# Kernel tuning notes

Hardware: AMD Instinct MI355X
Metric: run time of the kernel (lower is better)

The kernel has to match this reference:

```python
import jax, jax.numpy as jnp
import numpy as np

N_NODES = 50000
N_EDGES = 800000
D_IN = 128
D_OUT = 128


def setup_inputs() -> dict:
    key = jax.random.key(0)
    k1, k2, k3, k4, k5 = jax.random.split(key, 5)
    # xavier-uniform-like scale for the two linear layers (gain for relu ~ sqrt(2))
    bound = float(np.sqrt(2.0) * np.sqrt(6.0 / (D_IN + D_OUT)))
    return {
        "feat": jax.random.normal(k1, (N_NODES, D_IN), dtype=jnp.float32),
        "w_neigh": jax.random.uniform(k2, (D_OUT, D_IN), minval=-bound, maxval=bound, dtype=jnp.float32),
        "w_self": jax.random.uniform(k3, (D_OUT, D_IN), minval=-bound, maxval=bound, dtype=jnp.float32),
        "b_self": jnp.zeros((D_OUT,), dtype=jnp.float32),
        "rows": jax.random.randint(k4, (N_EDGES,), 0, N_NODES, dtype=jnp.int32),  # src node per edge
        "cols": jax.random.randint(k5, (N_EDGES,), 0, N_NODES, dtype=jnp.int32),  # dst node per edge
    }


def reference(feat, w_neigh, w_self, b_self, rows, cols):
    n = feat.shape[0]
    # srcdata = fc_neigh(feat): [N, D_OUT]
    srcdata = feat @ w_neigh.T
    # deg[j] = A.sum(0)[j] = in-degree of destination j (column sums)
    deg = jax.ops.segment_sum(jnp.ones_like(cols, dtype=feat.dtype), cols, num_segments=n)
    # dstdata = (A @ diag(deg)^-1).T @ srcdata  ==  mean over incoming src neighbors
    agg = jax.ops.segment_sum(srcdata[rows], cols, num_segments=n)  # [N, D_OUT]
    dstdata = agg / jnp.where(deg > 0, deg, 1.0)[:, None]
    # rst = fc_self(h_self) + dstdata
    return feat @ w_self.T + b_self + dstdata
```

## Files before the change

kernel.cpp:

```cpp
#include <hip/hip_runtime.h>
#include <hip/hip_bf16.h>

#define D 128
#define CAP 64

typedef __attribute__((ext_vector_type(8))) short bf16x8;
typedef __attribute__((ext_vector_type(4))) float floatx4;

__device__ __forceinline__ unsigned short f2bf(float f) {
    unsigned int u = __float_as_uint(f);
    return (unsigned short)((u + 0x7fffu + ((u >> 16) & 1u)) >> 16);
}

__global__ __launch_bounds__(256) void zero_kernel(int* __restrict__ p, int n) {
    int i = blockIdx.x * 256 + threadIdx.x;
    if (i < n) p[i] = 0;
}

__global__ __launch_bounds__(256) void prep_fill_kernel(
    const float* __restrict__ feat,
    const float* __restrict__ w_self,
    const float* __restrict__ w_neigh,
    const int* __restrict__ rows,
    const int* __restrict__ cols,
    unsigned short* __restrict__ feat_h,
    unsigned short* __restrict__ ws_h,
    unsigned short* __restrict__ wn_h,
    int* __restrict__ cursor,
    unsigned short* __restrict__ slots,
    int n_nodes, int n_edges)
{
    const int b = blockIdx.x;
    const int tid = threadIdx.x;
    const int role = b % 3;

    if (role < 2) {
        int pb = (b / 3) * 2 + role;
        int i  = pb * 256 + tid;
        if (i < n_nodes * 32) {
            float4 v = *(const float4*)&feat[(long long)4 * i];
            ushort4 o;
            o.x = f2bf(v.x); o.y = f2bf(v.y); o.z = f2bf(v.z); o.w = f2bf(v.w);
            *(ushort4*)&feat_h[(long long)4 * i] = o;
        }
    } else {
        int fb = b / 3;
        int e  = fb * 256 + tid;
        if (e < n_edges) {
            int c = cols[e];
            int p = atomicAdd(&cursor[c], 1);
            if (p < CAP) slots[c * CAP + p] = (unsigned short)rows[e];
        }
        if (fb < 32) {
            int i = fb * 256 + tid;
            int j = i & 4095;
            const float* src = (i < 4096) ? w_self : w_neigh;
            unsigned short* dst = (i < 4096) ? ws_h : wn_h;
            float4 v = *(const float4*)&src[4 * j];
            ushort4 o;
            o.x = f2bf(v.x); o.y = f2bf(v.y); o.z = f2bf(v.z); o.w = f2bf(v.w);
            *(ushort4*)&dst[4 * j] = o;
        }
    }
}

__global__ __launch_bounds__(256) void agg_kernel(
    const unsigned short* __restrict__ feat_h,
    const int* __restrict__ cursor,
    const unsigned short* __restrict__ slots,
    unsigned short* __restrict__ agg_h,
    int n_nodes)
{
    int gid = blockIdx.x * 256 + threadIdx.x;
    int node = gid >> 4;
    if (node >= n_nodes) return;
    int q = gid & 15;

    int deg = cursor[node];
    if (deg > CAP) deg = CAP;
    const unsigned short* slot = slots + (long long)node * CAP;

    float acc[8] = {0.f, 0.f, 0.f, 0.f, 0.f, 0.f, 0.f, 0.f};
    if (deg > 0) {
        int r = slot[0];
        for (int k = 0; k < deg; ++k) {
            int rn = (k + 1 < deg) ? (int)slot[k + 1] : 0;
            uint4 v = *(const uint4*)&feat_h[(long long)r * D + q * 8];
            acc[0] += __uint_as_float(v.x << 16);
            acc[1] += __uint_as_float(v.x & 0xffff0000u);
            acc[2] += __uint_as_float(v.y << 16);
            acc[3] += __uint_as_float(v.y & 0xffff0000u);
            acc[4] += __uint_as_float(v.z << 16);
            acc[5] += __uint_as_float(v.z & 0xffff0000u);
            acc[6] += __uint_as_float(v.w << 16);
            acc[7] += __uint_as_float(v.w & 0xffff0000u);
            r = rn;
        }
    }
    float inv = (deg > 0) ? 1.0f / (float)deg : 0.0f;

    ushort4 o0, o1;
    o0.x = f2bf(acc[0] * inv); o0.y = f2bf(acc[1] * inv);
    o0.z = f2bf(acc[2] * inv); o0.w = f2bf(acc[3] * inv);
    o1.x = f2bf(acc[4] * inv); o1.y = f2bf(acc[5] * inv);
    o1.z = f2bf(acc[6] * inv); o1.w = f2bf(acc[7] * inv);
    *(ushort4*)&agg_h[(long long)node * D + q * 8] = o0;
    *(ushort4*)&agg_h[(long long)node * D + q * 8 + 4] = o1;
}

__global__ __launch_bounds__(256) void gemm_mfma(
    const unsigned short* __restrict__ feat_h,
    const unsigned short* __restrict__ agg_h,
    const unsigned short* __restrict__ ws_h,
    const unsigned short* __restrict__ wn_h,
    const float* __restrict__ b_self,
    float* __restrict__ out,
    int n_nodes)
{
    const int tid  = threadIdx.x;
    const int wave = tid >> 6;
    const int lane = tid & 63;
    const int m    = lane & 15;
    const int quad = lane >> 4;
    const int row0 = blockIdx.x * 128 + wave * 32;
    const int kq   = quad * 8;

    floatx4 acc[8][2];
    #pragma unroll
    for (int nt = 0; nt < 8; ++nt)
        #pragma unroll
        for (int h = 0; h < 2; ++h)
            acc[nt][h] = (floatx4){0.f, 0.f, 0.f, 0.f};

    int r0 = row0 + m;      if (r0 > n_nodes - 1) r0 = n_nodes - 1;
    int r1 = row0 + 16 + m; if (r1 > n_nodes - 1) r1 = n_nodes - 1;

    #pragma unroll
    for (int phase = 0; phase < 2; ++phase) {
        const unsigned short* A = phase ? agg_h : feat_h;
        const unsigned short* B = phase ? wn_h : ws_h;
        #pragma unroll
        for (int kt = 0; kt < 4; ++kt) {
            const int k = kt * 32 + kq;
            bf16x8 a0 = *(const bf16x8*)&A[(long long)r0 * D + k];
            bf16x8 a1 = *(const bf16x8*)&A[(long long)r1 * D + k];
            #pragma unroll
            for (int nt = 0; nt < 8; ++nt) {
                bf16x8 b = *(const bf16x8*)&B[(nt * 16 + m) * D + k];
                acc[nt][0] = __builtin_amdgcn_mfma_f32_16x16x32_bf16(a0, b, acc[nt][0], 0, 0, 0);
                acc[nt][1] = __builtin_amdgcn_mfma_f32_16x16x32_bf16(a1, b, acc[nt][1], 0, 0, 0);
            }
        }
    }

    #pragma unroll
    for (int nt = 0; nt < 8; ++nt) {
        int col = nt * 16 + m;
        float bias = b_self[col];
        #pragma unroll
        for (int h = 0; h < 2; ++h) {
            #pragma unroll
            for (int r = 0; r < 4; ++r) {
                int row = row0 + h * 16 + quad * 4 + r;
                if (row < n_nodes)
                    out[(long long)row * D + col] = acc[nt][h][r] + bias;
            }
        }
    }
}

extern "C" void kernel_launch(void* const* d_in, const int* in_sizes, int n_in,
                              void* d_out, int out_size, void* d_ws, size_t ws_size,
                              hipStream_t stream) {
    const float* feat    = (const float*)d_in[0];
    const float* w_neigh = (const float*)d_in[1];
    const float* w_self  = (const float*)d_in[2];
    const float* b_self  = (const float*)d_in[3];
    const int*   rows    = (const int*)d_in[4];
    const int*   cols    = (const int*)d_in[5];
    float* out = (float*)d_out;

    const int n_nodes = in_sizes[0] / D;
    const int n_edges = in_sizes[4];

    unsigned short* feat_h = (unsigned short*)d_ws;
    unsigned short* agg_h  = feat_h + (size_t)n_nodes * D;
    unsigned short* slots  = agg_h + (size_t)n_nodes * D;
    int* cursor = (int*)(slots + (size_t)n_nodes * CAP);
    unsigned short* ws_h = (unsigned short*)(cursor + n_nodes);
    unsigned short* wn_h = ws_h + 16384;

    zero_kernel<<<(n_nodes + 255) / 256, 256, 0, stream>>>(cursor, n_nodes);

    int nblocks = (n_nodes * 32 + 255) / 256 + (n_edges + 255) / 256;
    prep_fill_kernel<<<nblocks, 256, 0, stream>>>(
        feat, w_self, w_neigh, rows, cols,
        feat_h, ws_h, wn_h, cursor, slots, n_nodes, n_edges);

    agg_kernel<<<(n_nodes * 16 + 255) / 256, 256, 0, stream>>>(
        feat_h, cursor, slots, agg_h, n_nodes);

    gemm_mfma<<<(n_nodes + 127) / 128, 256, 0, stream>>>(
        feat_h, agg_h, ws_h, wn_h, b_self, out, n_nodes);
}
```

Measured before the change: 195.4 us.

## Fuse neighbor mean aggregation into the MFMA GEMM via shared-memory tile

Merges the aggregation and GEMM kernels into one. Each block first gathers the mean of neighbor features for 64 nodes into LDS, then runs the self and neighbor MFMA GEMMs, with the aggregated tile read straight from LDS. This removes the global round trip for the bf16 agg buffer and one kernel launch. In exchange, each node's gather now uses 4 threads instead of 16, which lowers memory-level parallelism for the gather and raises register pressure. The GEMM tile also shrinks to 16 rows per wave.

```diff
diff --git a/kernel.cpp b/kernel.cpp
--- a/kernel.cpp
+++ b/kernel.cpp
@@ -3,6 +3,7 @@
 
 #define D 128
 #define CAP 64
+#define TILE 64
 
 typedef __attribute__((ext_vector_type(8))) short bf16x8;
 typedef __attribute__((ext_vector_type(4))) float floatx4;
@@ -64,92 +65,108 @@
     }
 }
 
-__global__ __launch_bounds__(256) void agg_kernel(
+__global__ __launch_bounds__(256, 4) void agg_gemm_kernel(
     const unsigned short* __restrict__ feat_h,
     const int* __restrict__ cursor,
     const unsigned short* __restrict__ slots,
-    unsigned short* __restrict__ agg_h,
-    int n_nodes)
-{
-    int gid = blockIdx.x * 256 + threadIdx.x;
-    int node = gid >> 4;
-    if (node >= n_nodes) return;
-    int q = gid & 15;
-
-    int deg = cursor[node];
-    if (deg > CAP) deg = CAP;
-    const unsigned short* slot = slots + (long long)node * CAP;
-
-    float acc[8] = {0.f, 0.f, 0.f, 0.f, 0.f, 0.f, 0.f, 0.f};
-    if (deg > 0) {
-        int r = slot[0];
-        for (int k = 0; k < deg; ++k) {
-            int rn = (k + 1 < deg) ? (int)slot[k + 1] : 0;
-            uint4 v = *(const uint4*)&feat_h[(long long)r * D + q * 8];
-            acc[0] += __uint_as_float(v.x << 16);
-            acc[1] += __uint_as_float(v.x & 0xffff0000u);
-            acc[2] += __uint_as_float(v.y << 16);
-            acc[3] += __uint_as_float(v.y & 0xffff0000u);
-            acc[4] += __uint_as_float(v.z << 16);
-            acc[5] += __uint_as_float(v.z & 0xffff0000u);
-            acc[6] += __uint_as_float(v.w << 16);
-            acc[7] += __uint_as_float(v.w & 0xffff0000u);
-            r = rn;
-        }
-    }
-    float inv = (deg > 0) ? 1.0f / (float)deg : 0.0f;
-
-    ushort4 o0, o1;
-    o0.x = f2bf(acc[0] * inv); o0.y = f2bf(acc[1] * inv);
-    o0.z = f2bf(acc[2] * inv); o0.w = f2bf(acc[3] * inv);
-    o1.x = f2bf(acc[4] * inv); o1.y = f2bf(acc[5] * inv);
-    o1.z = f2bf(acc[6] * inv); o1.w = f2bf(acc[7] * inv);
-    *(ushort4*)&agg_h[(long long)node * D + q * 8] = o0;
-    *(ushort4*)&agg_h[(long long)node * D + q * 8 + 4] = o1;
-}
-
-__global__ __launch_bounds__(256) void gemm_mfma(
-    const unsigned short* __restrict__ feat_h,
-    const unsigned short* __restrict__ agg_h,
     const unsigned short* __restrict__ ws_h,
     const unsigned short* __restrict__ wn_h,
     const float* __restrict__ b_self,
     float* __restrict__ out,
     int n_nodes)
 {
+    __shared__ unsigned short s_agg[TILE][136];
+
     const int tid  = threadIdx.x;
-    const int wave = tid >> 6;
-    const int lane = tid & 63;
-    const int m    = lane & 15;
-    const int quad = lane >> 4;
-    const int row0 = blockIdx.x * 128 + wave * 32;
-    const int kq   = quad * 8;
-
-    floatx4 acc[8][2];
-    #pragma unroll
-    for (int nt = 0; nt < 8; ++nt)
-        #pragma unroll
-        for (int h = 0; h < 2; ++h)
-            acc[nt][h] = (floatx4){0.f, 0.f, 0.f, 0.f};
-
-    int r0 = row0 + m;      if (r0 > n_nodes - 1) r0 = n_nodes - 1;
-    int r1 = row0 + 16 + m; if (r1 > n_nodes - 1) r1 = n_nodes - 1;
-
-    #pragma unroll
-    for (int phase = 0; phase < 2; ++phase) {
-        const unsigned short* A = phase ? agg_h : feat_h;
-        const unsigned short* B = phase ? wn_h : ws_h;
-        #pragma unroll
-        for (int kt = 0; kt < 4; ++kt) {
-            const int k = kt * 32 + kq;
-            bf16x8 a0 = *(const bf16x8*)&A[(long long)r0 * D + k];
-            bf16x8 a1 = *(const bf16x8*)&A[(long long)r1 * D + k];
+    const int row0 = blockIdx.x * TILE;
+
+    {
+        const int ln   = tid & 3;
+        const int nl   = tid >> 2;
+        const int node = row0 + nl;
+
+        float acc[32];
+        #pragma unroll
+        for (int i = 0; i < 32; ++i) acc[i] = 0.f;
+
+        int deg = 0;
+        if (node < n_nodes) {
+            deg = cursor[node];
+            if (deg > CAP) deg = CAP;
+            const unsigned short* slot = slots + (long long)node * CAP;
+            for (int k = 0; k < deg; ++k) {
+                int r = slot[k];
+                const unsigned short* base = feat_h + (long long)r * D + ln * 32;
+                uint4 v0 = *(const uint4*)(base + 0);
+                uint4 v1 = *(const uint4*)(base + 8);
+                uint4 v2 = *(const uint4*)(base + 16);
+                uint4 v3 = *(const uint4*)(base + 24);
+                const uint4 vv[4] = {v0, v1, v2, v3};
+                #pragma unroll
+                for (int c = 0; c < 4; ++c) {
+                    acc[c * 8 + 0] += __uint_as_float(vv[c].x << 16);
+                    acc[c * 8 + 1] += __uint_as_float(vv[c].x & 0xffff0000u);
+                    acc[c * 8 + 2] += __uint_as_float(vv[c].y << 16);
+                    acc[c * 8 + 3] += __uint_as_float(vv[c].y & 0xffff0000u);
+                    acc[c * 8 + 4] += __uint_as_float(vv[c].z << 16);
+                    acc[c * 8 + 5] += __uint_as_float(vv[c].z & 0xffff0000u);
+                    acc[c * 8 + 6] += __uint_as_float(vv[c].w << 16);
+                    acc[c * 8 + 7] += __uint_as_float(vv[c].w & 0xffff0000u);
+                }
+            }
+            float inv = (deg > 0) ? 1.0f / (float)deg : 0.0f;
             #pragma unroll
-            for (int nt = 0; nt < 8; ++nt) {
-                bf16x8 b = *(const bf16x8*)&B[(nt * 16 + m) * D + k];
-                acc[nt][0] = __builtin_amdgcn_mfma_f32_16x16x32_bf16(a0, b, acc[nt][0], 0, 0, 0);
-                acc[nt][1] = __builtin_amdgcn_mfma_f32_16x16x32_bf16(a1, b, acc[nt][1], 0, 0, 0);
+            for (int c = 0; c < 4; ++c) {
+                ushort4 o0, o1;
+                o0.x = f2bf(acc[c * 8 + 0] * inv); o0.y = f2bf(acc[c * 8 + 1] * inv);
+                o0.z = f2bf(acc[c * 8 + 2] * inv); o0.w = f2bf(acc[c * 8 + 3] * inv);
+                o1.x = f2bf(acc[c * 8 + 4] * inv); o1.y = f2bf(acc[c * 8 + 5] * inv);
+                o1.z = f2bf(acc[c * 8 + 6] * inv); o1.w = f2bf(acc[c * 8 + 7] * inv);
+                *(ushort4*)&s_agg[nl][ln * 32 + c * 8]     = o0;
+                *(ushort4*)&s_agg[nl][ln * 32 + c * 8 + 4] = o1;
             }
+        } else {
+            #pragma unroll
+            for (int c = 0; c < 4; ++c) {
+                *(ushort4*)&s_agg[nl][ln * 32 + c * 8]     = (ushort4){0,0,0,0};
+                *(ushort4*)&s_agg[nl][ln * 32 + c * 8 + 4] = (ushort4){0,0,0,0};
+            }
+        }
+    }
+    __syncthreads();
+
+    const int wave  = tid >> 6;
+    const int lane  = tid & 63;
+    const int m     = lane & 15;
+    const int quad  = lane >> 4;
+    const int kq    = quad * 8;
+    const int rbase = row0 + wave * 16;
+
+    floatx4 gacc[8];
+    #pragma unroll
+    for (int nt = 0; nt < 8; ++nt) gacc[nt] = (floatx4){0.f, 0.f, 0.f, 0.f};
+
+    int rA = rbase + m;
+    if (rA > n_nodes - 1) rA = n_nodes - 1;
+
+    #pragma unroll
+    for (int kt = 0; kt < 4; ++kt) {
+        const int k = kt * 32 + kq;
+        bf16x8 a = *(const bf16x8*)&feat_h[(long long)rA * D + k];
+        #pragma unroll
+        for (int nt = 0; nt < 8; ++nt) {
+            bf16x8 b = *(const bf16x8*)&ws_h[(nt * 16 + m) * D + k];
+            gacc[nt] = __builtin_amdgcn_mfma_f32_16x16x32_bf16(a, b, gacc[nt], 0, 0, 0);
+        }
+    }
+    #pragma unroll
+    for (int kt = 0; kt < 4; ++kt) {
+        const int k = kt * 32 + kq;
+        bf16x8 a = *(const bf16x8*)&s_agg[wave * 16 + m][k];
+        #pragma unroll
+        for (int nt = 0; nt < 8; ++nt) {
+            bf16x8 b = *(const bf16x8*)&wn_h[(nt * 16 + m) * D + k];
+            gacc[nt] = __builtin_amdgcn_mfma_f32_16x16x32_bf16(a, b, gacc[nt], 0, 0, 0);
         }
     }
 
@@ -158,13 +175,10 @@
         int col = nt * 16 + m;
         float bias = b_self[col];
         #pragma unroll
-        for (int h = 0; h < 2; ++h) {
-            #pragma unroll
-            for (int r = 0; r < 4; ++r) {
-                int row = row0 + h * 16 + quad * 4 + r;
-                if (row < n_nodes)
-                    out[(long long)row * D + col] = acc[nt][h][r] + bias;
-            }
+        for (int r = 0; r < 4; ++r) {
+            int row = rbase + quad * 4 + r;
+            if (row < n_nodes)
+                out[(long long)row * D + col] = gacc[nt][r] + bias;
         }
     }
 }
@@ -184,8 +198,7 @@
     const int n_edges = in_sizes[4];
 
     unsigned short* feat_h = (unsigned short*)d_ws;
-    unsigned short* agg_h  = feat_h + (size_t)n_nodes * D;
-    unsigned short* slots  = agg_h + (size_t)n_nodes * D;
+    unsigned short* slots  = feat_h + (size_t)n_nodes * D;
     int* cursor = (int*)(slots + (size_t)n_nodes * CAP);
     unsigned short* ws_h = (unsigned short*)(cursor + n_nodes);
     unsigned short* wn_h = ws_h + 16384;
@@ -197,9 +210,6 @@
         feat, w_self, w_neigh, rows, cols,
         feat_h, ws_h, wn_h, cursor, slots, n_nodes, n_edges);
 
-    agg_kernel<<<(n_nodes * 16 + 255) / 256, 256, 0, stream>>>(
-        feat_h, cursor, slots, agg_h, n_nodes);
-
-    gemm_mfma<<<(n_nodes + 127) / 128, 256, 0, stream>>>(
-        feat_h, agg_h, ws_h, wn_h, b_self, out, n_nodes);
-}
+    agg_gemm_kernel<<<(n_nodes + TILE - 1) / TILE, 256, 0, stream>>>(
+        feat_h, cursor, slots, ws_h, wn_h, b_self, out, n_nodes);
+}
```

New measurement: 193.4 us. Within noise of the previous version (-1.0%).
